# Kernel tuning notes

Hardware: AMD Instinct MI355X
Metric: run time of the kernel (lower is better)

## Reference

```python
import jax, jax.numpy as jnp
import numpy as np

IN_C = 256
KEY_C = 256
VAL_C = 256
HEADS = 8


def setup_inputs() -> dict:
    key = jax.random.key(0)
    ks = jax.random.split(key, 9)
    s = 0.02
    return {
        "x": jax.random.normal(ks[0], (4, 8192, IN_C), dtype=jnp.float32),
        "Wk": jax.random.normal(ks[1], (KEY_C, IN_C), dtype=jnp.float32) * s,
        "bk": jax.random.normal(ks[2], (KEY_C,), dtype=jnp.float32) * s,
        "Wq": jax.random.normal(ks[3], (KEY_C, IN_C), dtype=jnp.float32) * s,
        "bq": jax.random.normal(ks[4], (KEY_C,), dtype=jnp.float32) * s,
        "Wv": jax.random.normal(ks[5], (VAL_C, IN_C), dtype=jnp.float32) * s,
        "bv": jax.random.normal(ks[6], (VAL_C,), dtype=jnp.float32) * s,
        "Wr": jax.random.normal(ks[7], (IN_C, VAL_C), dtype=jnp.float32) * s,
        "br": jax.random.normal(ks[8], (IN_C,), dtype=jnp.float32) * s,
    }


def reference(x, Wk, bk, Wq, bq, Wv, bv, Wr, br):
    n, N, c = x.shape
    # Faithful to torch: reshape (NOT transpose) of (n, N, c) into (n, c, N)
    xi = x.reshape(n, c, N)
    # 1x1 convs == channel-mixing matmuls over the token axis
    K = jnp.einsum('oc,ncs->nos', Wk, xi) + bk[None, :, None]
    Q = jnp.einsum('oc,ncs->nos', Wq, xi) + bq[None, :, None]
    V = jnp.einsum('oc,ncs->nos', Wv, xi) + bv[None, :, None]
    dk = KEY_C // HEADS
    dv = VAL_C // HEADS
    Kh = K.reshape(n, HEADS, dk, N)
    Qh = Q.reshape(n, HEADS, dk, N)
    Vh = V.reshape(n, HEADS, dv, N)
    # keys: softmax over tokens (dim=2); queries: softmax over head key channels (dim=1)
    Kh = jax.nn.softmax(Kh, axis=3)
    Qh = jax.nn.softmax(Qh, axis=2)
    # context = K @ V^T : [n, H, dk, dv]
    ctx = jnp.einsum('nhks,nhvs->nhkv', Kh, Vh)
    # attended = context^T @ Q : [n, H, dv, N]
    att = jnp.einsum('nhkv,nhks->nhvs', ctx, Qh)
    agg = att.reshape(n, VAL_C, N)
    rep = jnp.einsum('ov,nvs->nos', Wr, agg) + br[None, :, None]
    out = rep + xi  # residual in (n, c, N) layout
    return jnp.transpose(out, (0, 2, 1))  # (n, N, c)
```

## Files before the change

kernel.cpp:

```cpp
#include <hip/hip_runtime.h>

#define NTOK 8192
#define NCH  256
#define TT   64
#define XTP  264
#define EKP  72

typedef unsigned short u16;
typedef __attribute__((ext_vector_type(8))) short bf16x8;
typedef __attribute__((ext_vector_type(4))) float f32x4;
typedef __attribute__((ext_vector_type(8))) unsigned short u16x8;
typedef __attribute__((ext_vector_type(4))) unsigned short u16x4;

__device__ __forceinline__ float b2f(u16 h){
  union{unsigned u; float f;} x; x.u = ((unsigned)h) << 16; return x.f;
}
__device__ __forceinline__ u16 f2b(float f){
  union{float f; unsigned u;} x; x.f = f;
  unsigned u = x.u;
  return (u16)((u + 0x7FFFu + ((u >> 16) & 1u)) >> 16);
}
__device__ __forceinline__ f32x4 mfma16(bf16x8 a, bf16x8 b, f32x4 c){
  return __builtin_amdgcn_mfma_f32_16x16x32_bf16(a, b, c, 0, 0, 0);
}

__device__ __forceinline__ void stage_xtile(const float* __restrict__ xb,
                                            u16* scratch, u16* dst, int t)
{
  #pragma unroll
  for (int i = 0; i < 4; ++i) {
    int ch = i * 64 + (t >> 3);
    int tk = (t & 7) * 8;
    const float* p = xb + (size_t)ch * NTOK + tk;
    float4 v0 = *(const float4*)p;
    float4 v1 = *(const float4*)(p + 4);
    u16x8 pk;
    pk[0]=f2b(v0.x); pk[1]=f2b(v0.y); pk[2]=f2b(v0.z); pk[3]=f2b(v0.w);
    pk[4]=f2b(v1.x); pk[5]=f2b(v1.y); pk[6]=f2b(v1.z); pk[7]=f2b(v1.w);
    *(u16x8*)&scratch[ch * EKP + tk] = pk;
  }
  __syncthreads();
  #pragma unroll
  for (int p = 0; p < 4; ++p) {
    int idx = p * 512 + t;
    int tok = idx & 63;
    int ch = (idx >> 6) * 8;
    u16x8 o;
    #pragma unroll
    for (int j = 0; j < 8; ++j) o[j] = scratch[(ch + j) * EKP + tok];
    *(u16x8*)&dst[tok * XTP + ch] = o;
  }
}

__global__ __launch_bounds__(256)
void k_prep(const float* __restrict__ Wk, const float* __restrict__ Wq,
            const float* __restrict__ Wv, const float* __restrict__ Wr,
            u16* __restrict__ wbf)
{
  const int t = threadIdx.x, bid = blockIdx.x;
  const int mat = bid >> 4;
  const float* src = (mat == 0) ? Wk : (mat == 1) ? Wq : (mat == 2) ? Wv : Wr;
  u16* dst = wbf + mat * 65536;
  const int base = (bid & 15) * 4096 + t * 16;
  #pragma unroll
  for (int i = 0; i < 4; ++i) {
    float4 v = *(const float4*)(src + base + i * 4);
    u16x4 pk; pk[0]=f2b(v.x); pk[1]=f2b(v.y); pk[2]=f2b(v.z); pk[3]=f2b(v.w);
    *(u16x4*)(dst + base + i * 4) = pk;
  }
}

__global__ __launch_bounds__(512, 4)
void k_ctx(const float* __restrict__ x, const u16* __restrict__ wbf,
           const float* __restrict__ bk, const float* __restrict__ bv,
           u16* __restrict__ xT,
           u16* __restrict__ ctxPart, float* __restrict__ denomPart)
{
  __shared__ u16 bufA[NCH * EKP];
  __shared__ u16 ekb[NCH * EKP];

  const int t = threadIdx.x;
  const int b = blockIdx.x >> 7, g = blockIdx.x & 127;
  const int w = t >> 6, lane = t & 63;
  const int l15 = lane & 15, quad = lane >> 4;
  const u16* Wkb = wbf;
  const u16* Wvb = wbf + 2 * 65536;

  stage_xtile(x + (size_t)b * NCH * NTOK + g * TT, ekb, bufA, t);
  __syncthreads();

  {
    u16* dst = xT + ((size_t)(b * NTOK + g * TT) << 8);
    #pragma unroll
    for (int i = 0; i < 4; ++i) {
      int f = i * 4096 + t * 8;
      int tok = f >> 8, ch = f & 255;
      *(u16x8*)(dst + f) = *(const u16x8*)&bufA[tok * XTP + ch];
    }
  }

  f32x4 acc[2][4];

  #pragma unroll
  for (int mi = 0; mi < 2; ++mi)
    #pragma unroll
    for (int nj = 0; nj < 4; ++nj) acc[mi][nj] = (f32x4)0.f;
  for (int k0 = 0; k0 < NCH; k0 += 32) {
    bf16x8 af[2], bx[4];
    #pragma unroll
    for (int mi = 0; mi < 2; ++mi)
      af[mi] = *(const bf16x8*)(Wkb + (size_t)(w * 32 + mi * 16 + l15) * NCH + k0 + quad * 8);
    #pragma unroll
    for (int nj = 0; nj < 4; ++nj)
      bx[nj] = *(const bf16x8*)&bufA[(nj * 16 + l15) * XTP + k0 + quad * 8];
    #pragma unroll
    for (int mi = 0; mi < 2; ++mi)
      #pragma unroll
      for (int nj = 0; nj < 4; ++nj) acc[mi][nj] = mfma16(af[mi], bx[nj], acc[mi][nj]);
  }
  #pragma unroll
  for (int mi = 0; mi < 2; ++mi) {
    float4 bb = *(const float4*)(bk + w * 32 + mi * 16 + quad * 4);
    #pragma unroll
    for (int nj = 0; nj < 4; ++nj) {
      int tok = nj * 16 + l15, chb = w * 32 + mi * 16 + quad * 4;
      ekb[(chb + 0) * EKP + tok] = f2b(__expf(acc[mi][nj][0] + bb.x));
      ekb[(chb + 1) * EKP + tok] = f2b(__expf(acc[mi][nj][1] + bb.y));
      ekb[(chb + 2) * EKP + tok] = f2b(__expf(acc[mi][nj][2] + bb.z));
      ekb[(chb + 3) * EKP + tok] = f2b(__expf(acc[mi][nj][3] + bb.w));
    }
  }

  #pragma unroll
  for (int mi = 0; mi < 2; ++mi)
    #pragma unroll
    for (int nj = 0; nj < 4; ++nj) acc[mi][nj] = (f32x4)0.f;
  for (int k0 = 0; k0 < NCH; k0 += 32) {
    bf16x8 af[2], bx[4];
    #pragma unroll
    for (int mi = 0; mi < 2; ++mi)
      af[mi] = *(const bf16x8*)(Wvb + (size_t)(w * 32 + mi * 16 + l15) * NCH + k0 + quad * 8);
    #pragma unroll
    for (int nj = 0; nj < 4; ++nj)
      bx[nj] = *(const bf16x8*)&bufA[(nj * 16 + l15) * XTP + k0 + quad * 8];
    #pragma unroll
    for (int mi = 0; mi < 2; ++mi)
      #pragma unroll
      for (int nj = 0; nj < 4; ++nj) acc[mi][nj] = mfma16(af[mi], bx[nj], acc[mi][nj]);
  }
  __syncthreads();
  #pragma unroll
  for (int mi = 0; mi < 2; ++mi) {
    float4 bb = *(const float4*)(bv + w * 32 + mi * 16 + quad * 4);
    #pragma unroll
    for (int nj = 0; nj < 4; ++nj) {
      int tok = nj * 16 + l15, chb = w * 32 + mi * 16 + quad * 4;
      bufA[(chb + 0) * EKP + tok] = f2b(acc[mi][nj][0] + bb.x);
      bufA[(chb + 1) * EKP + tok] = f2b(acc[mi][nj][1] + bb.y);
      bufA[(chb + 2) * EKP + tok] = f2b(acc[mi][nj][2] + bb.z);
      bufA[(chb + 3) * EKP + tok] = f2b(acc[mi][nj][3] + bb.w);
    }
  }
  __syncthreads();

  f32x4 cacc[2][2];
  #pragma unroll
  for (int mi = 0; mi < 2; ++mi)
    #pragma unroll
    for (int nj = 0; nj < 2; ++nj) cacc[mi][nj] = (f32x4)0.f;
  #pragma unroll
  for (int kc = 0; kc < 2; ++kc) {
    bf16x8 ae[2], bvv[2];
    #pragma unroll
    for (int mi = 0; mi < 2; ++mi)
      ae[mi] = *(const bf16x8*)&ekb[(w * 32 + mi * 16 + l15) * EKP + kc * 32 + quad * 8];
    #pragma unroll
    for (int nj = 0; nj < 2; ++nj)
      bvv[nj] = *(const bf16x8*)&bufA[(w * 32 + nj * 16 + l15) * EKP + kc * 32 + quad * 8];
    #pragma unroll
    for (int mi = 0; mi < 2; ++mi)
      #pragma unroll
      for (int nj = 0; nj < 2; ++nj)
        cacc[mi][nj] = mfma16(ae[mi], bvv[nj], cacc[mi][nj]);
  }
  float dsum = 0.f;
  if (t < 256) {
    #pragma unroll
    for (int s = 0; s < TT; s += 8) {
      u16x8 v = *(const u16x8*)&ekb[t * EKP + s];
      #pragma unroll
      for (int j = 0; j < 8; ++j) dsum += b2f(v[j]);
    }
  }

  u16* cp = ctxPart + ((size_t)(b * 128 + g) << 13);
  #pragma unroll
  for (int mi = 0; mi < 2; ++mi)
    #pragma unroll
    for (int nj = 0; nj < 2; ++nj)
      #pragma unroll
      for (int r = 0; r < 4; ++r) {
        int e = ((w * 32 + mi * 16 + quad * 4 + r) << 5) + nj * 16 + l15;
        cp[e] = f2b(cacc[mi][nj][r]);
      }
  if (t < 256)
    denomPart[(size_t)(b * 128 + g) * 256 + t] = dsum;
}

__global__ __launch_bounds__(256)
void k_red(const u16* __restrict__ ctxPart, const float* __restrict__ denomPart,
           u16* __restrict__ ctxT, float* __restrict__ rdenomF)
{
  int i = blockIdx.x * 256 + threadIdx.x;
  if (i < 4096) {
    const int base = i * 8;
    const int b = base >> 13, e = base & 8191;
    const u16* p = ctxPart + (((size_t)b * 128) << 13) + e;
    float s[8];
    #pragma unroll
    for (int j = 0; j < 8; ++j) s[j] = 0.f;
    #pragma unroll 4
    for (int g = 0; g < 128; ++g) {
      u16x8 v = *(const u16x8*)(p + ((size_t)g << 13));
      #pragma unroll
      for (int j = 0; j < 8; ++j) s[j] += b2f(v[j]);
    }
    const int hh = e >> 10, kk = (e >> 5) & 31, vchb = e & 31;
    #pragma unroll
    for (int j = 0; j < 8; ++j)
      ctxT[(((b * 8 + hh) * 32 + vchb + j) << 5) + kk] = f2b(s[j]);
  } else if (i < 5120) {
    int j = i - 4096, b = j >> 8, ch = j & 255;
    const float* p = denomPart + (size_t)(b * 128) * 256 + ch;
    float s = 0.f;
    #pragma unroll 8
    for (int g = 0; g < 128; ++g) s += p[(size_t)g << 8];
    rdenomF[j] = 1.0f / s;
  }
}

__global__ __launch_bounds__(512, 4)
void k_out(const u16* __restrict__ xT, const u16* __restrict__ wbf,
           const float* __restrict__ bq, const float* __restrict__ br,
           const u16* __restrict__ ctxT, const float* __restrict__ rdenomF,
           float* __restrict__ out)
{
  __shared__ u16 xs[TT * XTP];
  __shared__ u16 qs[TT * XTP];

  const int t = threadIdx.x;
  const int b = blockIdx.x >> 7, g = blockIdx.x & 127;
  const int w = t >> 6, lane = t & 63;
  const int l15 = lane & 15, quad = lane >> 4;
  const u16* Wqb = wbf + 65536;
  const u16* Wrb = wbf + 3 * 65536;

  {
    const u16* src = xT + ((size_t)(b * NTOK + g * TT) << 8);
    #pragma unroll
    for (int i = 0; i < 4; ++i) {
      int f = i * 4096 + t * 8;
      int tok = f >> 8, ch = f & 255;
      *(u16x8*)&xs[tok * XTP + ch] = *(const u16x8*)(src + f);
    }
  }
  __syncthreads();

  bf16x8 ac[2];
  #pragma unroll
  for (int mi = 0; mi < 2; ++mi)
    ac[mi] = *(const bf16x8*)(ctxT + (((size_t)(b * 8 + w) * 32 + mi * 16 + l15) << 5) + quad * 8);

  f32x4 acc[2][4];
  #pragma unroll
  for (int mi = 0; mi < 2; ++mi)
    #pragma unroll
    for (int nj = 0; nj < 4; ++nj) acc[mi][nj] = (f32x4)0.f;
  for (int k0 = 0; k0 < NCH; k0 += 32) {
    bf16x8 af[2], bx[4];
    #pragma unroll
    for (int mi = 0; mi < 2; ++mi)
      af[mi] = *(const bf16x8*)(Wqb + (size_t)(w * 32 + mi * 16 + l15) * NCH + k0 + quad * 8);
    #pragma unroll
    for (int nj = 0; nj < 4; ++nj)
      bx[nj] = *(const bf16x8*)&xs[(nj * 16 + l15) * XTP + k0 + quad * 8];
    #pragma unroll
    for (int mi = 0; mi < 2; ++mi)
      #pragma unroll
      for (int nj = 0; nj < 4; ++nj) acc[mi][nj] = mfma16(af[mi], bx[nj], acc[mi][nj]);
  }
  #pragma unroll
  for (int mi = 0; mi < 2; ++mi) {
    float4 bb = *(const float4*)(bq + w * 32 + mi * 16 + quad * 4);
    #pragma unroll
    for (int nj = 0; nj < 4; ++nj) {
      acc[mi][nj][0] = __expf(acc[mi][nj][0] + bb.x);
      acc[mi][nj][1] = __expf(acc[mi][nj][1] + bb.y);
      acc[mi][nj][2] = __expf(acc[mi][nj][2] + bb.z);
      acc[mi][nj][3] = __expf(acc[mi][nj][3] + bb.w);
    }
  }
  float inv[4];
  #pragma unroll
  for (int nj = 0; nj < 4; ++nj) {
    float s = 0.f;
    #pragma unroll
    for (int mi = 0; mi < 2; ++mi)
      #pragma unroll
      for (int r = 0; r < 4; ++r) s += acc[mi][nj][r];
    s += __shfl_xor(s, 16);
    s += __shfl_xor(s, 32);
    inv[nj] = 1.0f / s;
  }
  #pragma unroll
  for (int mi = 0; mi < 2; ++mi) {
    float4 rd = *(const float4*)(rdenomF + b * 256 + w * 32 + mi * 16 + quad * 4);
    #pragma unroll
    for (int nj = 0; nj < 4; ++nj) {
      u16x4 pk;
      pk[0] = f2b(acc[mi][nj][0] * inv[nj] * rd.x);
      pk[1] = f2b(acc[mi][nj][1] * inv[nj] * rd.y);
      pk[2] = f2b(acc[mi][nj][2] * inv[nj] * rd.z);
      pk[3] = f2b(acc[mi][nj][3] * inv[nj] * rd.w);
      *(u16x4*)&qs[(nj * 16 + l15) * XTP + w * 32 + mi * 16 + quad * 4] = pk;
    }
  }
  __syncthreads();

  f32x4 aacc[2][4];
  {
    #pragma unroll
    for (int nj = 0; nj < 4; ++nj) {
      bf16x8 bqf = *(const bf16x8*)&qs[(nj * 16 + l15) * XTP + w * 32 + quad * 8];
      #pragma unroll
      for (int mi = 0; mi < 2; ++mi)
        aacc[mi][nj] = mfma16(ac[mi], bqf, (f32x4)0.f);
    }
  }
  #pragma unroll
  for (int mi = 0; mi < 2; ++mi)
    #pragma unroll
    for (int nj = 0; nj < 4; ++nj) {
      u16x4 pk;
      pk[0] = f2b(aacc[mi][nj][0]);
      pk[1] = f2b(aacc[mi][nj][1]);
      pk[2] = f2b(aacc[mi][nj][2]);
      pk[3] = f2b(aacc[mi][nj][3]);
      *(u16x4*)&qs[(nj * 16 + l15) * XTP + w * 32 + mi * 16 + quad * 4] = pk;
    }
  __syncthreads();

  #pragma unroll
  for (int mi = 0; mi < 2; ++mi)
    #pragma unroll
    for (int nj = 0; nj < 4; ++nj) acc[mi][nj] = (f32x4)0.f;
  for (int k0 = 0; k0 < NCH; k0 += 32) {
    bf16x8 af[2], bx[4];
    #pragma unroll
    for (int mi = 0; mi < 2; ++mi)
      af[mi] = *(const bf16x8*)(Wrb + (size_t)(w * 32 + mi * 16 + l15) * NCH + k0 + quad * 8);
    #pragma unroll
    for (int nj = 0; nj < 4; ++nj)
      bx[nj] = *(const bf16x8*)&qs[(nj * 16 + l15) * XTP + k0 + quad * 8];
    #pragma unroll
    for (int mi = 0; mi < 2; ++mi)
      #pragma unroll
      for (int nj = 0; nj < 4; ++nj) acc[mi][nj] = mfma16(af[mi], bx[nj], acc[mi][nj]);
  }
  #pragma unroll
  for (int mi = 0; mi < 2; ++mi) {
    float4 bb = *(const float4*)(br + w * 32 + mi * 16 + quad * 4);
    #pragma unroll
    for (int nj = 0; nj < 4; ++nj) {
      int tok = nj * 16 + l15;
      u16x4 rx = *(const u16x4*)&xs[tok * XTP + w * 32 + mi * 16 + quad * 4];
      float4 o;
      o.x = acc[mi][nj][0] + bb.x + b2f(rx[0]);
      o.y = acc[mi][nj][1] + bb.y + b2f(rx[1]);
      o.z = acc[mi][nj][2] + bb.z + b2f(rx[2]);
      o.w = acc[mi][nj][3] + bb.w + b2f(rx[3]);
      *(float4*)(out + (((size_t)(b * NTOK + g * TT + tok)) << 8) + w * 32 + mi * 16 + quad * 4) = o;
    }
  }
}

extern "C" void kernel_launch(void* const* d_in, const int* in_sizes, int n_in,
                              void* d_out, int out_size, void* d_ws, size_t ws_size,
                              hipStream_t stream) {
  const float* x  = (const float*)d_in[0];
  const float* Wk = (const float*)d_in[1];
  const float* bk = (const float*)d_in[2];
  const float* Wq = (const float*)d_in[3];
  const float* bq = (const float*)d_in[4];
  const float* Wv = (const float*)d_in[5];
  const float* bv = (const float*)d_in[6];
  const float* Wr = (const float*)d_in[7];
  const float* br = (const float*)d_in[8];
  float* out = (float*)d_out;

  char* wsb = (char*)d_ws;
  u16*   ctxPart   = (u16*)wsb;
  float* denomPart = (float*)(wsb + 8388608);
  u16*   ctxT      = (u16*)(wsb + 8912896);
  float* rdenomF   = (float*)(wsb + 8978432);
  u16*   wbf       = (u16*)(wsb + 8982528);
  u16*   xT        = (u16*)(wsb + 9506816);

  hipLaunchKernelGGL(k_prep, dim3(64), dim3(256), 0, stream,
                     Wk, Wq, Wv, Wr, wbf);
  hipLaunchKernelGGL(k_ctx, dim3(512), dim3(512), 0, stream,
                     x, wbf, bk, bv, xT, ctxPart, denomPart);
  hipLaunchKernelGGL(k_red, dim3(20), dim3(256), 0, stream,
                     ctxPart, denomPart, ctxT, rdenomF);
  hipLaunchKernelGGL(k_out, dim3(512), dim3(512), 0, stream,
                     xT, wbf, bq, br, ctxT, rdenomF, out);
}
```

Before: 154.5 us.

## Halve token tile to 32, drop bf16 xT intermediate, re-stage x in output kernel

The per-block token tile shrinks from 64 to 32, so k_ctx and k_out launch twice as many blocks with smaller shared-memory footprints and a higher occupancy bound. The bf16 transposed copy of x (xT) is no longer written by k_ctx. Instead k_out reloads fp32 x and transposes it itself. This removes one 16 MB write and read at the cost of a second 32 MB fp32 read. The number of partial context and denominator slices doubles, so ctxPart traffic doubles and the 20-block reduction kernel must sum 256 partials instead of 128.

```diff
diff --git a/kernel.cpp b/kernel.cpp
--- a/kernel.cpp
+++ b/kernel.cpp
@@ -2,9 +2,9 @@
 
 #define NTOK 8192
 #define NCH  256
-#define TT   64
+#define TT   32
 #define XTP  264
-#define EKP  72
+#define EK2  40
 
 typedef unsigned short u16;
 typedef __attribute__((ext_vector_type(8))) short bf16x8;
@@ -24,30 +24,30 @@
   return __builtin_amdgcn_mfma_f32_16x16x32_bf16(a, b, c, 0, 0, 0);
 }
 
-__device__ __forceinline__ void stage_xtile(const float* __restrict__ xb,
-                                            u16* scratch, u16* dst, int t)
-{
-  #pragma unroll
-  for (int i = 0; i < 4; ++i) {
-    int ch = i * 64 + (t >> 3);
-    int tk = (t & 7) * 8;
+__device__ __forceinline__ void stage_xtile32(const float* __restrict__ xb,
+                                              u16* scratch, u16* dst, int t)
+{
+  #pragma unroll
+  for (int i = 0; i < 2; ++i) {
+    int ch = i * 128 + (t >> 2);
+    int tk = (t & 3) * 8;
     const float* p = xb + (size_t)ch * NTOK + tk;
     float4 v0 = *(const float4*)p;
     float4 v1 = *(const float4*)(p + 4);
     u16x8 pk;
     pk[0]=f2b(v0.x); pk[1]=f2b(v0.y); pk[2]=f2b(v0.z); pk[3]=f2b(v0.w);
     pk[4]=f2b(v1.x); pk[5]=f2b(v1.y); pk[6]=f2b(v1.z); pk[7]=f2b(v1.w);
-    *(u16x8*)&scratch[ch * EKP + tk] = pk;
-  }
-  __syncthreads();
-  #pragma unroll
-  for (int p = 0; p < 4; ++p) {
-    int idx = p * 512 + t;
-    int tok = idx & 63;
-    int ch = (idx >> 6) * 8;
+    *(u16x8*)&scratch[ch * EK2 + tk] = pk;
+  }
+  __syncthreads();
+  #pragma unroll
+  for (int p2 = 0; p2 < 2; ++p2) {
+    int idx = p2 * 512 + t;
+    int tok = idx & 31;
+    int ch = (idx >> 5) * 8;
     u16x8 o;
     #pragma unroll
-    for (int j = 0; j < 8; ++j) o[j] = scratch[(ch + j) * EKP + tok];
+    for (int j = 0; j < 8; ++j) o[j] = scratch[(ch + j) * EK2 + tok];
     *(u16x8*)&dst[tok * XTP + ch] = o;
   }
 }
@@ -70,130 +70,114 @@
   }
 }
 
-__global__ __launch_bounds__(512, 4)
+__global__ __launch_bounds__(512, 8)
 void k_ctx(const float* __restrict__ x, const u16* __restrict__ wbf,
            const float* __restrict__ bk, const float* __restrict__ bv,
-           u16* __restrict__ xT,
            u16* __restrict__ ctxPart, float* __restrict__ denomPart)
 {
-  __shared__ u16 bufA[NCH * EKP];
-  __shared__ u16 ekb[NCH * EKP];
+  __shared__ u16 bufA[NCH * EK2];
+  __shared__ u16 ekb[NCH * EK2];
 
   const int t = threadIdx.x;
-  const int b = blockIdx.x >> 7, g = blockIdx.x & 127;
+  const int b = blockIdx.x >> 8, g = blockIdx.x & 255;
   const int w = t >> 6, lane = t & 63;
   const int l15 = lane & 15, quad = lane >> 4;
   const u16* Wkb = wbf;
   const u16* Wvb = wbf + 2 * 65536;
 
-  stage_xtile(x + (size_t)b * NCH * NTOK + g * TT, ekb, bufA, t);
-  __syncthreads();
-
+  stage_xtile32(x + (size_t)b * NCH * NTOK + g * TT, ekb, bufA, t);
+  __syncthreads();
+
+  f32x4 acc[2][2];
+
+  #pragma unroll
+  for (int mi = 0; mi < 2; ++mi)
+    #pragma unroll
+    for (int nj = 0; nj < 2; ++nj) acc[mi][nj] = (f32x4)0.f;
+  for (int k0 = 0; k0 < NCH; k0 += 32) {
+    bf16x8 af[2], bx[2];
+    #pragma unroll
+    for (int mi = 0; mi < 2; ++mi)
+      af[mi] = *(const bf16x8*)(Wkb + (size_t)(w * 32 + mi * 16 + l15) * NCH + k0 + quad * 8);
+    #pragma unroll
+    for (int nj = 0; nj < 2; ++nj)
+      bx[nj] = *(const bf16x8*)&bufA[(nj * 16 + l15) * XTP + k0 + quad * 8];
+    #pragma unroll
+    for (int mi = 0; mi < 2; ++mi)
+      #pragma unroll
+      for (int nj = 0; nj < 2; ++nj) acc[mi][nj] = mfma16(af[mi], bx[nj], acc[mi][nj]);
+  }
+  #pragma unroll
+  for (int mi = 0; mi < 2; ++mi) {
+    float4 bb = *(const float4*)(bk + w * 32 + mi * 16 + quad * 4);
+    #pragma unroll
+    for (int nj = 0; nj < 2; ++nj) {
+      int tok = nj * 16 + l15, chb = w * 32 + mi * 16 + quad * 4;
+      ekb[(chb + 0) * EK2 + tok] = f2b(__expf(acc[mi][nj][0] + bb.x));
+      ekb[(chb + 1) * EK2 + tok] = f2b(__expf(acc[mi][nj][1] + bb.y));
+      ekb[(chb + 2) * EK2 + tok] = f2b(__expf(acc[mi][nj][2] + bb.z));
+      ekb[(chb + 3) * EK2 + tok] = f2b(__expf(acc[mi][nj][3] + bb.w));
+    }
+  }
+
+  #pragma unroll
+  for (int mi = 0; mi < 2; ++mi)
+    #pragma unroll
+    for (int nj = 0; nj < 2; ++nj) acc[mi][nj] = (f32x4)0.f;
+  for (int k0 = 0; k0 < NCH; k0 += 32) {
+    bf16x8 af[2], bx[2];
+    #pragma unroll
+    for (int mi = 0; mi < 2; ++mi)
+      af[mi] = *(const bf16x8*)(Wvb + (size_t)(w * 32 + mi * 16 + l15) * NCH + k0 + quad * 8);
+    #pragma unroll
+    for (int nj = 0; nj < 2; ++nj)
+      bx[nj] = *(const bf16x8*)&bufA[(nj * 16 + l15) * XTP + k0 + quad * 8];
+    #pragma unroll
+    for (int mi = 0; mi < 2; ++mi)
+      #pragma unroll
+      for (int nj = 0; nj < 2; ++nj) acc[mi][nj] = mfma16(af[mi], bx[nj], acc[mi][nj]);
+  }
+  __syncthreads();
+  #pragma unroll
+  for (int mi = 0; mi < 2; ++mi) {
+    float4 bb = *(const float4*)(bv + w * 32 + mi * 16 + quad * 4);
+    #pragma unroll
+    for (int nj = 0; nj < 2; ++nj) {
+      int tok = nj * 16 + l15, chb = w * 32 + mi * 16 + quad * 4;
+      bufA[(chb + 0) * EK2 + tok] = f2b(acc[mi][nj][0] + bb.x);
+      bufA[(chb + 1) * EK2 + tok] = f2b(acc[mi][nj][1] + bb.y);
+      bufA[(chb + 2) * EK2 + tok] = f2b(acc[mi][nj][2] + bb.z);
+      bufA[(chb + 3) * EK2 + tok] = f2b(acc[mi][nj][3] + bb.w);
+    }
+  }
+  __syncthreads();
+
+  f32x4 cacc[2][2];
   {
-    u16* dst = xT + ((size_t)(b * NTOK + g * TT) << 8);
-    #pragma unroll
-    for (int i = 0; i < 4; ++i) {
-      int f = i * 4096 + t * 8;
-      int tok = f >> 8, ch = f & 255;
-      *(u16x8*)(dst + f) = *(const u16x8*)&bufA[tok * XTP + ch];
-    }
-  }
-
-  f32x4 acc[2][4];
-
-  #pragma unroll
-  for (int mi = 0; mi < 2; ++mi)
-    #pragma unroll
-    for (int nj = 0; nj < 4; ++nj) acc[mi][nj] = (f32x4)0.f;
-  for (int k0 = 0; k0 < NCH; k0 += 32) {
-    bf16x8 af[2], bx[4];
-    #pragma unroll
-    for (int mi = 0; mi < 2; ++mi)
-      af[mi] = *(const bf16x8*)(Wkb + (size_t)(w * 32 + mi * 16 + l15) * NCH + k0 + quad * 8);
-    #pragma unroll
-    for (int nj = 0; nj < 4; ++nj)
-      bx[nj] = *(const bf16x8*)&bufA[(nj * 16 + l15) * XTP + k0 + quad * 8];
-    #pragma unroll
-    for (int mi = 0; mi < 2; ++mi)
-      #pragma unroll
-      for (int nj = 0; nj < 4; ++nj) acc[mi][nj] = mfma16(af[mi], bx[nj], acc[mi][nj]);
-  }
-  #pragma unroll
-  for (int mi = 0; mi < 2; ++mi) {
-    float4 bb = *(const float4*)(bk + w * 32 + mi * 16 + quad * 4);
-    #pragma unroll
-    for (int nj = 0; nj < 4; ++nj) {
-      int tok = nj * 16 + l15, chb = w * 32 + mi * 16 + quad * 4;
-      ekb[(chb + 0) * EKP + tok] = f2b(__expf(acc[mi][nj][0] + bb.x));
-      ekb[(chb + 1) * EKP + tok] = f2b(__expf(acc[mi][nj][1] + bb.y));
-      ekb[(chb + 2) * EKP + tok] = f2b(__expf(acc[mi][nj][2] + bb.z));
-      ekb[(chb + 3) * EKP + tok] = f2b(__expf(acc[mi][nj][3] + bb.w));
-    }
-  }
-
-  #pragma unroll
-  for (int mi = 0; mi < 2; ++mi)
-    #pragma unroll
-    for (int nj = 0; nj < 4; ++nj) acc[mi][nj] = (f32x4)0.f;
-  for (int k0 = 0; k0 < NCH; k0 += 32) {
-    bf16x8 af[2], bx[4];
-    #pragma unroll
-    for (int mi = 0; mi < 2; ++mi)
-      af[mi] = *(const bf16x8*)(Wvb + (size_t)(w * 32 + mi * 16 + l15) * NCH + k0 + quad * 8);
-    #pragma unroll
-    for (int nj = 0; nj < 4; ++nj)
-      bx[nj] = *(const bf16x8*)&bufA[(nj * 16 + l15) * XTP + k0 + quad * 8];
-    #pragma unroll
-    for (int mi = 0; mi < 2; ++mi)
-      #pragma unroll
-      for (int nj = 0; nj < 4; ++nj) acc[mi][nj] = mfma16(af[mi], bx[nj], acc[mi][nj]);
-  }
-  __syncthreads();
-  #pragma unroll
-  for (int mi = 0; mi < 2; ++mi) {
-    float4 bb = *(const float4*)(bv + w * 32 + mi * 16 + quad * 4);
-    #pragma unroll
-    for (int nj = 0; nj < 4; ++nj) {
-      int tok = nj * 16 + l15, chb = w * 32 + mi * 16 + quad * 4;
-      bufA[(chb + 0) * EKP + tok] = f2b(acc[mi][nj][0] + bb.x);
-      bufA[(chb + 1) * EKP + tok] = f2b(acc[mi][nj][1] + bb.y);
-      bufA[(chb + 2) * EKP + tok] = f2b(acc[mi][nj][2] + bb.z);
-      bufA[(chb + 3) * EKP + tok] = f2b(acc[mi][nj][3] + bb.w);
-    }
-  }
-  __syncthreads();
-
-  f32x4 cacc[2][2];
-  #pragma unroll
-  for (int mi = 0; mi < 2; ++mi)
-    #pragma unroll
-    for (int nj = 0; nj < 2; ++nj) cacc[mi][nj] = (f32x4)0.f;
-  #pragma unroll
-  for (int kc = 0; kc < 2; ++kc) {
     bf16x8 ae[2], bvv[2];
     #pragma unroll
     for (int mi = 0; mi < 2; ++mi)
-      ae[mi] = *(const bf16x8*)&ekb[(w * 32 + mi * 16 + l15) * EKP + kc * 32 + quad * 8];
-    #pragma unroll
-    for (int nj = 0; nj < 2; ++nj)
-      bvv[nj] = *(const bf16x8*)&bufA[(w * 32 + nj * 16 + l15) * EKP + kc * 32 + quad * 8];
+      ae[mi] = *(const bf16x8*)&ekb[(w * 32 + mi * 16 + l15) * EK2 + quad * 8];
+    #pragma unroll
+    for (int nj = 0; nj < 2; ++nj)
+      bvv[nj] = *(const bf16x8*)&bufA[(w * 32 + nj * 16 + l15) * EK2 + quad * 8];
     #pragma unroll
     for (int mi = 0; mi < 2; ++mi)
       #pragma unroll
       for (int nj = 0; nj < 2; ++nj)
-        cacc[mi][nj] = mfma16(ae[mi], bvv[nj], cacc[mi][nj]);
+        cacc[mi][nj] = mfma16(ae[mi], bvv[nj], (f32x4)0.f);
   }
   float dsum = 0.f;
   if (t < 256) {
     #pragma unroll
     for (int s = 0; s < TT; s += 8) {
-      u16x8 v = *(const u16x8*)&ekb[t * EKP + s];
+      u16x8 v = *(const u16x8*)&ekb[t * EK2 + s];
       #pragma unroll
       for (int j = 0; j < 8; ++j) dsum += b2f(v[j]);
     }
   }
 
-  u16* cp = ctxPart + ((size_t)(b * 128 + g) << 13);
+  u16* cp = ctxPart + ((size_t)(b * 256 + g) << 13);
   #pragma unroll
   for (int mi = 0; mi < 2; ++mi)
     #pragma unroll
@@ -204,7 +188,7 @@
         cp[e] = f2b(cacc[mi][nj][r]);
       }
   if (t < 256)
-    denomPart[(size_t)(b * 128 + g) * 256 + t] = dsum;
+    denomPart[(size_t)(b * 256 + g) * 256 + t] = dsum;
 }
 
 __global__ __launch_bounds__(256)
@@ -215,12 +199,12 @@
   if (i < 4096) {
     const int base = i * 8;
     const int b = base >> 13, e = base & 8191;
-    const u16* p = ctxPart + (((size_t)b * 128) << 13) + e;
+    const u16* p = ctxPart + (((size_t)b * 256) << 13) + e;
     float s[8];
     #pragma unroll
     for (int j = 0; j < 8; ++j) s[j] = 0.f;
     #pragma unroll 4
-    for (int g = 0; g < 128; ++g) {
+    for (int g = 0; g < 256; ++g) {
       u16x8 v = *(const u16x8*)(p + ((size_t)g << 13));
       #pragma unroll
       for (int j = 0; j < 8; ++j) s[j] += b2f(v[j]);
@@ -231,39 +215,31 @@
       ctxT[(((b * 8 + hh) * 32 + vchb + j) << 5) + kk] = f2b(s[j]);
   } else if (i < 5120) {
     int j = i - 4096, b = j >> 8, ch = j & 255;
-    const float* p = denomPart + (size_t)(b * 128) * 256 + ch;
+    const float* p = denomPart + (size_t)(b * 256) * 256 + ch;
     float s = 0.f;
     #pragma unroll 8
-    for (int g = 0; g < 128; ++g) s += p[(size_t)g << 8];
+    for (int g = 0; g < 256; ++g) s += p[(size_t)g << 8];
     rdenomF[j] = 1.0f / s;
   }
 }
 
-__global__ __launch_bounds__(512, 4)
-void k_out(const u16* __restrict__ xT, const u16* __restrict__ wbf,
+__global__ __launch_bounds__(512, 8)
+void k_out(const float* __restrict__ x, const u16* __restrict__ wbf,
            const float* __restrict__ bq, const float* __restrict__ br,
            const u16* __restrict__ ctxT, const float* __restrict__ rdenomF,
            float* __restrict__ out)
 {
   __shared__ u16 xs[TT * XTP];
-  __shared__ u16 qs[TT * XTP];
+  __shared__ u16 qs[NCH * EK2];
 
   const int t = threadIdx.x;
-  const int b = blockIdx.x >> 7, g = blockIdx.x & 127;
+  const int b = blockIdx.x >> 8, g = blockIdx.x & 255;
   const int w = t >> 6, lane = t & 63;
   const int l15 = lane & 15, quad = lane >> 4;
   const u16* Wqb = wbf + 65536;
   const u16* Wrb = wbf + 3 * 65536;
 
-  {
-    const u16* src = xT + ((size_t)(b * NTOK + g * TT) << 8);
-    #pragma unroll
-    for (int i = 0; i < 4; ++i) {
-      int f = i * 4096 + t * 8;
-      int tok = f >> 8, ch = f & 255;
-      *(u16x8*)&xs[tok * XTP + ch] = *(const u16x8*)(src + f);
-    }
-  }
+  stage_xtile32(x + (size_t)b * NCH * NTOK + g * TT, qs, xs, t);
   __syncthreads();
 
   bf16x8 ac[2];
@@ -271,38 +247,38 @@
   for (int mi = 0; mi < 2; ++mi)
     ac[mi] = *(const bf16x8*)(ctxT + (((size_t)(b * 8 + w) * 32 + mi * 16 + l15) << 5) + quad * 8);
 
-  f32x4 acc[2][4];
-  #pragma unroll
-  for (int mi = 0; mi < 2; ++mi)
-    #pragma unroll
-    for (int nj = 0; nj < 4; ++nj) acc[mi][nj] = (f32x4)0.f;
+  f32x4 acc[2][2];
+  #pragma unroll
+  for (int mi = 0; mi < 2; ++mi)
+    #pragma unroll
+    for (int nj = 0; nj < 2; ++nj) acc[mi][nj] = (f32x4)0.f;
   for (int k0 = 0; k0 < NCH; k0 += 32) {
-    bf16x8 af[2], bx[4];
+    bf16x8 af[2], bx[2];
     #pragma unroll
     for (int mi = 0; mi < 2; ++mi)
       af[mi] = *(const bf16x8*)(Wqb + (size_t)(w * 32 + mi * 16 + l15) * NCH + k0 + quad * 8);
     #pragma unroll
-    for (int nj = 0; nj < 4; ++nj)
+    for (int nj = 0; nj < 2; ++nj)
       bx[nj] = *(const bf16x8*)&xs[(nj * 16 + l15) * XTP + k0 + quad * 8];
     #pragma unroll
     for (int mi = 0; mi < 2; ++mi)
       #pragma unroll
-      for (int nj = 0; nj < 4; ++nj) acc[mi][nj] = mfma16(af[mi], bx[nj], acc[mi][nj]);
+      for (int nj = 0; nj < 2; ++nj) acc[mi][nj] = mfma16(af[mi], bx[nj], acc[mi][nj]);
   }
   #pragma unroll
   for (int mi = 0; mi < 2; ++mi) {
     float4 bb = *(const float4*)(bq + w * 32 + mi * 16 + quad * 4);
     #pragma unroll
-    for (int nj = 0; nj < 4; ++nj) {
+    for (int nj = 0; nj < 2; ++nj) {
       acc[mi][nj][0] = __expf(acc[mi][nj][0] + bb.x);
       acc[mi][nj][1] = __expf(acc[mi][nj][1] + bb.y);
       acc[mi][nj][2] = __expf(acc[mi][nj][2] + bb.z);
       acc[mi][nj][3] = __expf(acc[mi][nj][3] + bb.w);
     }
   }
-  float inv[4];
-  #pragma unroll
-  for (int nj = 0; nj < 4; ++nj) {
+  float inv[2];
+  #pragma unroll
+  for (int nj = 0; nj < 2; ++nj) {
     float s = 0.f;
     #pragma unroll
     for (int mi = 0; mi < 2; ++mi)
@@ -316,7 +292,7 @@
   for (int mi = 0; mi < 2; ++mi) {
     float4 rd = *(const float4*)(rdenomF + b * 256 + w * 32 + mi * 16 + quad * 4);
     #pragma unroll
-    for (int nj = 0; nj < 4; ++nj) {
+    for (int nj = 0; nj < 2; ++nj) {
       u16x4 pk;
       pk[0] = f2b(acc[mi][nj][0] * inv[nj] * rd.x);
       pk[1] = f2b(acc[mi][nj][1] * inv[nj] * rd.y);
@@ -327,10 +303,10 @@
   }
   __syncthreads();
 
-  f32x4 aacc[2][4];
+  f32x4 aacc[2][2];
   {
     #pragma unroll
-    for (int nj = 0; nj < 4; ++nj) {
+    for (int nj = 0; nj < 2; ++nj) {
       bf16x8 bqf = *(const bf16x8*)&qs[(nj * 16 + l15) * XTP + w * 32 + quad * 8];
       #pragma unroll
       for (int mi = 0; mi < 2; ++mi)
@@ -340,7 +316,7 @@
   #pragma unroll
   for (int mi = 0; mi < 2; ++mi)
     #pragma unroll
-    for (int nj = 0; nj < 4; ++nj) {
+    for (int nj = 0; nj < 2; ++nj) {
       u16x4 pk;
       pk[0] = f2b(aacc[mi][nj][0]);
       pk[1] = f2b(aacc[mi][nj][1]);
@@ -353,25 +329,25 @@
   #pragma unroll
   for (int mi = 0; mi < 2; ++mi)
     #pragma unroll
-    for (int nj = 0; nj < 4; ++nj) acc[mi][nj] = (f32x4)0.f;
+    for (int nj = 0; nj < 2; ++nj) acc[mi][nj] = (f32x4)0.f;
   for (int k0 = 0; k0 < NCH; k0 += 32) {
-    bf16x8 af[2], bx[4];
+    bf16x8 af[2], bx[2];
     #pragma unroll
     for (int mi = 0; mi < 2; ++mi)
       af[mi] = *(const bf16x8*)(Wrb + (size_t)(w * 32 + mi * 16 + l15) * NCH + k0 + quad * 8);
     #pragma unroll
-    for (int nj = 0; nj < 4; ++nj)
+    for (int nj = 0; nj < 2; ++nj)
       bx[nj] = *(const bf16x8*)&qs[(nj * 16 + l15) * XTP + k0 + quad * 8];
     #pragma unroll
     for (int mi = 0; mi < 2; ++mi)
       #pragma unroll
-      for (int nj = 0; nj < 4; ++nj) acc[mi][nj] = mfma16(af[mi], bx[nj], acc[mi][nj]);
+      for (int nj = 0; nj < 2; ++nj) acc[mi][nj] = mfma16(af[mi], bx[nj], acc[mi][nj]);
   }
   #pragma unroll
   for (int mi = 0; mi < 2; ++mi) {
     float4 bb = *(const float4*)(br + w * 32 + mi * 16 + quad * 4);
     #pragma unroll
-    for (int nj = 0; nj < 4; ++nj) {
+    for (int nj = 0; nj < 2; ++nj) {
       int tok = nj * 16 + l15;
       u16x4 rx = *(const u16x4*)&xs[tok * XTP + w * 32 + mi * 16 + quad * 4];
       float4 o;
@@ -400,18 +376,17 @@
 
   char* wsb = (char*)d_ws;
   u16*   ctxPart   = (u16*)wsb;
-  float* denomPart = (float*)(wsb + 8388608);
-  u16*   ctxT      = (u16*)(wsb + 8912896);
-  float* rdenomF   = (float*)(wsb + 8978432);
-  u16*   wbf       = (u16*)(wsb + 8982528);
-  u16*   xT        = (u16*)(wsb + 9506816);
+  float* denomPart = (float*)(wsb + 16777216);
+  u16*   ctxT      = (u16*)(wsb + 17825792);
+  float* rdenomF   = (float*)(wsb + 17891328);
+  u16*   wbf       = (u16*)(wsb + 17895424);
 
   hipLaunchKernelGGL(k_prep, dim3(64), dim3(256), 0, stream,
                      Wk, Wq, Wv, Wr, wbf);
-  hipLaunchKernelGGL(k_ctx, dim3(512), dim3(512), 0, stream,
-                     x, wbf, bk, bv, xT, ctxPart, denomPart);
+  hipLaunchKernelGGL(k_ctx, dim3(1024), dim3(512), 0, stream,
+                     x, wbf, bk, bv, ctxPart, denomPart);
   hipLaunchKernelGGL(k_red, dim3(20), dim3(256), 0, stream,
                      ctxPart, denomPart, ctxT, rdenomF);
-  hipLaunchKernelGGL(k_out, dim3(512), dim3(512), 0, stream,
-                     xT, wbf, bq, br, ctxT, rdenomF, out);
-}
+  hipLaunchKernelGGL(k_out, dim3(1024), dim3(512), 0, stream,
+                     x, wbf, bq, br, ctxT, rdenomF, out);
+}
```

After: 191.0 us. 1.24x slower.
